# Performance work log

Hardware: AMD Instinct MI355X
Metric: run time of the kernel (lower is better)

The kernel has to match this reference:

```python
import jax, jax.numpy as jnp
import numpy as np

EPS = 1e-5
GROUPS = 32


def setup_inputs() -> dict:
    key = jax.random.key(0)
    ks = jax.random.split(key, 3)
    B, C, H, W = 4, 256, 64, 64
    x = jax.random.normal(ks[0], (B, C, H, W), dtype=jnp.float32)
    gn_w = jnp.ones((C,), dtype=jnp.float32)
    gn_b = jnp.zeros((C,), dtype=jnp.float32)
    qkv_w = jax.random.normal(ks[1], (3 * C, C), dtype=jnp.float32) * (C ** -0.5)
    qkv_b = jnp.zeros((3 * C,), dtype=jnp.float32)
    proj_w = jax.random.normal(ks[2], (C, C), dtype=jnp.float32) * (C ** -0.5)
    proj_b = jnp.zeros((C,), dtype=jnp.float32)
    return {"x": x, "gn_w": gn_w, "gn_b": gn_b, "qkv_w": qkv_w,
            "qkv_b": qkv_b, "proj_w": proj_w, "proj_b": proj_b}


def reference(x, gn_w, gn_b, qkv_w, qkv_b, proj_w, proj_b):
    B, C, H, W = x.shape
    N = H * W
    # GroupNorm over (C//G, H, W) per group
    xg = x.reshape(B, GROUPS, -1)
    mean = xg.mean(axis=-1, keepdims=True)
    var = xg.var(axis=-1, keepdims=True)
    h = ((xg - mean) * jax.lax.rsqrt(var + EPS)).reshape(B, C, H, W)
    h = h * gn_w[None, :, None, None] + gn_b[None, :, None, None]
    # 1x1 conv QKV == channel GEMM
    hf = h.reshape(B, C, N)
    qkv = jnp.einsum('oc,bcn->bon', qkv_w, hf) + qkv_b[None, :, None]
    q, k, v = (qkv[:, :C], qkv[:, C:2 * C], qkv[:, 2 * C:])  # each [B,C,N]
    scale = C ** -0.5
    attn = jax.nn.softmax(jnp.einsum('bcn,bcm->bnm', q, k) * scale, axis=-1)
    out = jnp.einsum('bnm,bcm->bcn', attn, v)  # [B,C,N]
    y = jnp.einsum('oc,bcn->bon', proj_w, out) + proj_b[None, :, None]
    return x + y.reshape(B, C, H, W)
```

## Files before the change

### kernel.cpp

```cpp
#include <hip/hip_runtime.h>
#include <cstdint>
#include <cstddef>

typedef __attribute__((ext_vector_type(8))) short bf16x8;
typedef __attribute__((ext_vector_type(4))) short s16x4;
typedef __attribute__((ext_vector_type(2))) short s16x2;
typedef __attribute__((ext_vector_type(4))) float f32x4;
typedef __attribute__((ext_vector_type(16))) float f32x16;
typedef __attribute__((ext_vector_type(4))) unsigned u32x4;

#define DEVI static __device__ __forceinline__

DEVI short f2bf(float f){
  unsigned u = __builtin_bit_cast(unsigned, f);
  u += 0x7fffu + ((u >> 16) & 1u);
  return (short)(u >> 16);
}
DEVI float bf2f(short s){
  unsigned u = ((unsigned)(unsigned short)s) << 16;
  return __builtin_bit_cast(float, u);
}
DEVI unsigned pack_bf16_rne(float a, float b){
  unsigned ua = __builtin_bit_cast(unsigned, a);
  unsigned ub = __builtin_bit_cast(unsigned, b);
  ua += 0x7fffu + ((ua >> 16) & 1u);
  ub += 0x7fffu + ((ub >> 16) & 1u);
  return (ua >> 16) | (ub & 0xffff0000u);
}

DEVI f32x4 mfma16(bf16x8 a, bf16x8 b, f32x4 c){
  return __builtin_amdgcn_mfma_f32_16x16x32_bf16(a, b, c, 0, 0, 0);
}
DEVI f32x16 mfma32(bf16x8 a, bf16x8 b, f32x16 c){
  return __builtin_amdgcn_mfma_f32_32x32x16_bf16(a, b, c, 0, 0, 0);
}

#define QSC 0.09016844005555897f
#define FIXM 8.0f

__global__ __launch_bounds__(256) void k_conv(const float* __restrict__ wq, const float* __restrict__ wp,
                                              short* __restrict__ wqb, short* __restrict__ wpb){
  int t = blockIdx.x * 256 + threadIdx.x;
  for (int i = t; i < 768 * 256; i += 256 * 256) wqb[i] = f2bf(wq[i]);
  if (t < 256 * 256) wpb[t] = f2bf(wp[t]);
}

__global__ __launch_bounds__(256) void k_stats(const float* __restrict__ x, float2* __restrict__ st){
  int b = blockIdx.x >> 5, g = blockIdx.x & 31;
  const f32x4* p = (const f32x4*)(x + ((size_t)(b * 256 + g * 8)) * 4096);
  float s = 0.f, ss = 0.f;
  for (int i = threadIdx.x; i < 8192; i += 256){
    f32x4 v = p[i];
    s  += v[0] + v[1] + v[2] + v[3];
    ss += v[0]*v[0] + v[1]*v[1] + v[2]*v[2] + v[3]*v[3];
  }
  for (int d = 32; d; d >>= 1){ s += __shfl_down(s, d); ss += __shfl_down(ss, d); }
  __shared__ float a0[4], a1[4];
  int w = threadIdx.x >> 6;
  if ((threadIdx.x & 63) == 0){ a0[w] = s; a1[w] = ss; }
  __syncthreads();
  if (threadIdx.x == 0){
    s = a0[0] + a0[1] + a0[2] + a0[3];
    ss = a1[0] + a1[1] + a1[2] + a1[3];
    float mean = s * (1.f / 32768.f);
    float var = ss * (1.f / 32768.f) - mean * mean;
    st[blockIdx.x] = make_float2(mean, rsqrtf(var + 1e-5f));
  }
}

__global__ __launch_bounds__(256) void k_norm(const float* __restrict__ x, const float2* __restrict__ st,
                                              const float* __restrict__ gw, const float* __restrict__ gb,
                                              short* __restrict__ h_t){
  __shared__ short t[256][66];
  int b = blockIdx.x >> 6;
  int n0 = (blockIdx.x & 63) * 64;
  int tid = threadIdx.x;
  for (int r = 0; r < 16; ++r){
    int idx = tid + r * 256;
    int c = idx >> 4, ch = idx & 15;
    f32x4 v = *(const f32x4*)(x + ((size_t)(b * 256 + c)) * 4096 + n0 + ch * 4);
    float2 s = st[b * 32 + (c >> 3)];
    float wv = gw[c] * s.y;
    float bv = gb[c] - s.x * wv;
    s16x2 p0, p1;
    p0[0] = f2bf(v[0] * wv + bv); p0[1] = f2bf(v[1] * wv + bv);
    p1[0] = f2bf(v[2] * wv + bv); p1[1] = f2bf(v[3] * wv + bv);
    *(s16x2*)&t[c][ch * 4]     = p0;
    *(s16x2*)&t[c][ch * 4 + 2] = p1;
  }
  __syncthreads();
  for (int r = 0; r < 8; ++r){
    int idx = tid + r * 256;
    int n = idx >> 5, cc = idx & 31;
    bf16x8 pk;
    #pragma unroll
    for (int j = 0; j < 8; ++j) pk[j] = t[cc * 8 + j][n];
    *(bf16x8*)(h_t + ((size_t)(b * 4096 + n0 + n)) * 256 + cc * 8) = pk;
  }
}

__global__ __launch_bounds__(256) void k_gemm(const short* __restrict__ A,
                                              const short* __restrict__ Bsrc,
                                              const float* __restrict__ bias,
                                              int mtiles, int mode,
                                              short* __restrict__ q_t, short* __restrict__ k_t,
                                              short* __restrict__ v_,
                                              const float* __restrict__ xres, float* __restrict__ outp)
{
  __shared__ short a_s[128 * 72];
  __shared__ short b_s[128 * 72];
  int t = blockIdx.x;
  int mt = t % mtiles; t /= mtiles;
  int nt = t & 31; int b = t >> 5;
  int o0 = mt * 128, n0 = nt * 128;
  int tid = threadIdx.x;
  int lane = tid & 63, w = tid >> 6;
  int col = lane & 15, quad = lane >> 4;
  int wo = (w >> 1) * 64, wn = (w & 1) * 64;

  f32x4 acc[4][4];
  #pragma unroll
  for (int i = 0; i < 4; ++i)
    #pragma unroll
    for (int j = 0; j < 4; ++j)
      #pragma unroll
      for (int r = 0; r < 4; ++r) acc[i][j][r] = 0.f;

  for (int kk = 0; kk < 4; ++kk){
    int k0 = kk * 64;
    #pragma unroll
    for (int r = 0; r < 4; ++r){
      int idx = tid + r * 256;
      int row = idx >> 3, ch = idx & 7;
      *(bf16x8*)&a_s[row * 72 + ch * 8] = *(const bf16x8*)(A + (size_t)(o0 + row) * 256 + k0 + ch * 8);
      *(bf16x8*)&b_s[row * 72 + ch * 8] = *(const bf16x8*)(Bsrc + ((size_t)(b * 4096 + n0 + row)) * 256 + k0 + ch * 8);
    }
    __syncthreads();
    #pragma unroll
    for (int kc = 0; kc < 2; ++kc){
      bf16x8 af[4], bfr[4];
      #pragma unroll
      for (int i = 0; i < 4; ++i) af[i]  = *(bf16x8*)&a_s[(wo + i * 16 + col) * 72 + kc * 32 + quad * 8];
      #pragma unroll
      for (int j = 0; j < 4; ++j) bfr[j] = *(bf16x8*)&b_s[(wn + j * 16 + col) * 72 + kc * 32 + quad * 8];
      #pragma unroll
      for (int i = 0; i < 4; ++i)
        #pragma unroll
        for (int j = 0; j < 4; ++j)
          acc[i][j] = mfma16(af[i], bfr[j], acc[i][j]);
    }
    __syncthreads();
  }

  float bv[4][4];
  #pragma unroll
  for (int i = 0; i < 4; ++i)
    #pragma unroll
    for (int r = 0; r < 4; ++r) bv[i][r] = bias[o0 + wo + i * 16 + quad * 4 + r];

  if (mode == 0){
    int region = o0 >> 8;
    int obase = (o0 & 255) + wo;
    if (region < 2){
      short* dst = region ? k_t : q_t;
      float sc = region ? 1.0f : QSC;
      #pragma unroll
      for (int i = 0; i < 4; ++i)
        #pragma unroll
        for (int j = 0; j < 4; ++j){
          int n = n0 + wn + j * 16 + col;
          s16x4 pk;
          #pragma unroll
          for (int r = 0; r < 4; ++r) pk[r] = f2bf((acc[i][j][r] + bv[i][r]) * sc);
          *(s16x4*)(dst + ((size_t)(b * 4096 + n)) * 256 + obase + i * 16 + quad * 4) = pk;
        }
    } else {
      #pragma unroll
      for (int i = 0; i < 4; ++i)
        #pragma unroll
        for (int r = 0; r < 4; ++r){
          int oo = obase + i * 16 + quad * 4 + r;
          #pragma unroll
          for (int j = 0; j < 4; ++j){
            int n = n0 + wn + j * 16 + col;
            v_[((size_t)(b * 256 + oo)) * 4096 + n] = f2bf(acc[i][j][r] + bv[i][r]);
          }
        }
    }
  } else {
    #pragma unroll
    for (int i = 0; i < 4; ++i)
      #pragma unroll
      for (int r = 0; r < 4; ++r){
        int oo = o0 + wo + i * 16 + quad * 4 + r;
        #pragma unroll
        for (int j = 0; j < 4; ++j){
          int n = n0 + wn + j * 16 + col;
          size_t off = ((size_t)(b * 256 + oo)) * 4096 + n;
          outp[off] = xres[off] + acc[i][j][r] + bv[i][r];
        }
      }
  }
}

__global__ __launch_bounds__(256, 2) void k_attn(const short* __restrict__ q_t, const short* __restrict__ k_t,
                                                 const short* __restrict__ v_,
                                                 short* __restrict__ o_part, float* __restrict__ lsum)
{
  __shared__ short k_s[32 * 256];
  __shared__ short v_s[256 * 32];
  int idx = blockIdx.x;
  int qt = idx >> 4;
  int chunk = idx & 15;
  int b  = chunk >> 2;
  int ck = chunk & 3;
  int q0 = qt * 128;
  int tid = threadIdx.x, lane = tid & 63, w = tid >> 6;
  int col = lane & 31, h = lane >> 5;

  const short* qp = q_t + ((size_t)(b * 4096 + q0 + w * 32 + col)) * 256 + h * 8;
  bf16x8 qf[16];
  #pragma unroll
  for (int ks2 = 0; ks2 < 16; ++ks2) qf[ks2] = *(const bf16x8*)(qp + ks2 * 16);

  const short* kcb = k_t + ((size_t)(b * 4096 + ck * 1024)) * 256;
  const short* vcb = v_  + ((size_t)b) * 256 * 4096 + ck * 1024;

  int k_r = w * 8 + (lane >> 5);
  int k_p = lane & 31;
  int v_c = w * 64 + (lane >> 2);
  int v_p = lane & 3;

  f32x16 o_acc[8];
  #pragma unroll
  for (int ct = 0; ct < 8; ++ct)
    #pragma unroll
    for (int r = 0; r < 16; ++r) o_acc[ct][r] = 0.f;
  float l_acc = 0.f;

  #pragma unroll 1
  for (int it = 0; it < 32; ++it){
    int m0 = it * 32;
    bf16x8 kst[4], vst[4];
    #pragma unroll
    for (int i = 0; i < 4; ++i){
      kst[i] = *(const bf16x8*)(kcb + (size_t)(m0 + k_r + i * 2) * 256 + k_p * 8);
      vst[i] = *(const bf16x8*)(vcb + (size_t)(v_c + i * 16) * 4096 + m0 + v_p * 8);
    }
    if (it) __syncthreads();
    #pragma unroll
    for (int i = 0; i < 4; ++i){
      int r = k_r + i * 2;
      *(bf16x8*)&k_s[r * 256 + (k_p ^ (r & 7)) * 8] = kst[i];
      int c = v_c + i * 16;
      *(bf16x8*)&v_s[c * 32 + (v_p ^ ((c >> 1) & 3)) * 8] = vst[i];
    }
    __syncthreads();

    f32x16 s;
    #pragma unroll
    for (int r = 0; r < 16; ++r) s[r] = 0.f;
    #pragma unroll
    for (int ks2 = 0; ks2 < 16; ++ks2){
      bf16x8 kb = *(const bf16x8*)&k_s[col * 256 + (((ks2 * 2 + h) ^ (col & 7)) * 8)];
      s = mfma32(kb, qf[ks2], s);
    }

    bf16x8 pa0, pa1;
    {
      float p0 = __builtin_amdgcn_exp2f(s[0] - FIXM);
      float p1 = __builtin_amdgcn_exp2f(s[1] - FIXM);
      float p2 = __builtin_amdgcn_exp2f(s[2] - FIXM);
      float p3 = __builtin_amdgcn_exp2f(s[3] - FIXM);
      float p4 = __builtin_amdgcn_exp2f(s[4] - FIXM);
      float p5 = __builtin_amdgcn_exp2f(s[5] - FIXM);
      float p6 = __builtin_amdgcn_exp2f(s[6] - FIXM);
      float p7 = __builtin_amdgcn_exp2f(s[7] - FIXM);
      l_acc += p0 + p1 + p2 + p3 + p4 + p5 + p6 + p7;
      unsigned A0 = pack_bf16_rne(p0, p1), A1 = pack_bf16_rne(p2, p3);
      unsigned B0 = pack_bf16_rne(p4, p5), B1 = pack_bf16_rne(p6, p7);
      unsigned sA0 = __shfl_xor(A0, 32), sA1 = __shfl_xor(A1, 32);
      unsigned sB0 = __shfl_xor(B0, 32), sB1 = __shfl_xor(B1, 32);
      u32x4 w0;
      w0[0] = h ? sB0 : A0;  w0[1] = h ? sB1 : A1;
      w0[2] = h ? B0 : sA0;  w0[3] = h ? B1 : sA1;
      pa0 = __builtin_bit_cast(bf16x8, w0);
    }
    {
      float p0 = __builtin_amdgcn_exp2f(s[8]  - FIXM);
      float p1 = __builtin_amdgcn_exp2f(s[9]  - FIXM);
      float p2 = __builtin_amdgcn_exp2f(s[10] - FIXM);
      float p3 = __builtin_amdgcn_exp2f(s[11] - FIXM);
      float p4 = __builtin_amdgcn_exp2f(s[12] - FIXM);
      float p5 = __builtin_amdgcn_exp2f(s[13] - FIXM);
      float p6 = __builtin_amdgcn_exp2f(s[14] - FIXM);
      float p7 = __builtin_amdgcn_exp2f(s[15] - FIXM);
      l_acc += p0 + p1 + p2 + p3 + p4 + p5 + p6 + p7;
      unsigned C0 = pack_bf16_rne(p0, p1), C1 = pack_bf16_rne(p2, p3);
      unsigned D0 = pack_bf16_rne(p4, p5), D1 = pack_bf16_rne(p6, p7);
      unsigned sC0 = __shfl_xor(C0, 32), sC1 = __shfl_xor(C1, 32);
      unsigned sD0 = __shfl_xor(D0, 32), sD1 = __shfl_xor(D1, 32);
      u32x4 w1;
      w1[0] = h ? sD0 : C0;  w1[1] = h ? sD1 : C1;
      w1[2] = h ? D0 : sC0;  w1[3] = h ? D1 : sC1;
      pa1 = __builtin_bit_cast(bf16x8, w1);
    }

    #pragma unroll
    for (int ct = 0; ct < 8; ++ct){
      int c = ct * 32 + col;
      int sw = (c >> 1) & 3;
      bf16x8 vf0 = *(const bf16x8*)&v_s[c * 32 + ((h ^ sw) * 8)];
      bf16x8 vf1 = *(const bf16x8*)&v_s[c * 32 + (((2 + h) ^ sw) * 8)];
      o_acc[ct] = mfma32(pa0, vf0, o_acc[ct]);
      o_acc[ct] = mfma32(pa1, vf1, o_acc[ct]);
    }
  }

  short* op = o_part + (((size_t)(ck * 4 + b)) * 4096 + q0 + w * 32) * 256;
  #pragma unroll
  for (int r = 0; r < 16; ++r){
    int q = (r & 3) + 8 * (r >> 2) + 4 * h;
    #pragma unroll
    for (int ct = 0; ct < 8; ++ct)
      op[(size_t)q * 256 + ct * 32 + col] = f2bf(o_acc[ct][r]);
  }
  l_acc += __shfl_xor(l_acc, 32);
  if (h == 0)
    lsum[((size_t)(ck * 4 + b)) * 4096 + q0 + w * 32 + col] = l_acc;
}

__global__ __launch_bounds__(256) void k_comb(const short* __restrict__ o_part, const float* __restrict__ lsum,
                                              short* __restrict__ o_t)
{
  int t = blockIdx.x * 256 + threadIdx.x;
  int row = t >> 5;
  int c8 = (t & 31) * 8;
  float inv = 1.f / (lsum[row] + lsum[16384 + row] + lsum[2 * 16384 + row] + lsum[3 * 16384 + row]);
  size_t base = (size_t)row * 256 + c8;
  const size_t CS = (size_t)16384 * 256;
  bf16x8 a0 = *(const bf16x8*)(o_part + base);
  bf16x8 a1 = *(const bf16x8*)(o_part + CS + base);
  bf16x8 a2 = *(const bf16x8*)(o_part + 2 * CS + base);
  bf16x8 a3 = *(const bf16x8*)(o_part + 3 * CS + base);
  bf16x8 outv;
  #pragma unroll
  for (int j = 0; j < 8; ++j)
    outv[j] = f2bf((bf2f(a0[j]) + bf2f(a1[j]) + bf2f(a2[j]) + bf2f(a3[j])) * inv);
  *(bf16x8*)(o_t + base) = outv;
}

extern "C" void kernel_launch(void* const* d_in, const int* in_sizes, int n_in,
                              void* d_out, int out_size, void* d_ws, size_t ws_size,
                              hipStream_t stream)
{
  const float* x     = (const float*)d_in[0];
  const float* gw    = (const float*)d_in[1];
  const float* gb    = (const float*)d_in[2];
  const float* qkvw  = (const float*)d_in[3];
  const float* qkvb  = (const float*)d_in[4];
  const float* projw = (const float*)d_in[5];
  const float* projb = (const float*)d_in[6];
  float* out = (float*)d_out;

  char* ws = (char*)d_ws;
  float2* stats = (float2*)ws;
  short* wqb = (short*)(ws + 1024);
  short* wpb = (short*)(ws + 1024 + 393216);
  short* h_t = (short*)(ws + 1024 + 393216 + 131072);
  const size_t BIG = (size_t)4 * 4096 * 256;
  short* q_t = h_t + BIG;
  short* k_t = q_t + BIG;
  short* v_  = k_t + BIG;
  short* o_t = v_  + BIG;
  short* o_part = o_t + BIG;
  float* lsum = (float*)(o_part + 4 * BIG);

  k_conv <<<dim3(256),  dim3(256), 0, stream>>>(qkvw, projw, wqb, wpb);
  k_stats<<<dim3(128),  dim3(256), 0, stream>>>(x, stats);
  k_norm <<<dim3(256),  dim3(256), 0, stream>>>(x, stats, gw, gb, h_t);
  k_gemm <<<dim3(768),  dim3(256), 0, stream>>>(wqb, h_t, qkvb, 6, 0, q_t, k_t, v_,
                                                (const float*)nullptr, (float*)nullptr);
  k_attn <<<dim3(512),  dim3(256), 0, stream>>>(q_t, k_t, v_, o_part, lsum);
  k_comb <<<dim3(2048), dim3(256), 0, stream>>>(o_part, lsum, o_t);
  k_gemm <<<dim3(256),  dim3(256), 0, stream>>>(wpb, o_t, projb, 2, 1,
                                                (short*)nullptr, (short*)nullptr, (short*)nullptr,
                                                x, out);
}
```

Baseline: 205.0 us.

## Double-buffer attention K/V tiles with direct global-to-LDS loads

The attention kernel now stages K and V tiles straight from global memory into LDS with global_load_lds, into two ping-pong buffers, so loading tile it+1 overlaps compute on tile it. The swizzle moves from the LDS write side to the per-lane global source address. The QK^T MFMA chain is also split into two independent accumulators to shorten the dependency chain. LDS use doubles to 64KB per block, which may limit the two-blocks-per-CU occupancy target. It also relies on the async LDS loads having landed by the barrier, with no explicit vmcnt wait.

```diff
diff --git a/kernel.cpp b/kernel.cpp
--- a/kernel.cpp
+++ b/kernel.cpp
@@ -26,6 +26,10 @@
   ua += 0x7fffu + ((ua >> 16) & 1u);
   ub += 0x7fffu + ((ub >> 16) & 1u);
   return (ua >> 16) | (ub & 0xffff0000u);
+}
+DEVI void g2l16(const short* g, short* l){
+  __builtin_amdgcn_global_load_lds((const __attribute__((address_space(1))) void*)g,
+                                   (__attribute__((address_space(3))) void*)l, 16, 0, 0);
 }
 
 DEVI f32x4 mfma16(bf16x8 a, bf16x8 b, f32x4 c){
@@ -207,8 +211,8 @@
                                                  const short* __restrict__ v_,
                                                  short* __restrict__ o_part, float* __restrict__ lsum)
 {
-  __shared__ short k_s[32 * 256];
-  __shared__ short v_s[256 * 32];
+  __shared__ short k_s[2][32 * 256];
+  __shared__ short v_s[2][256 * 32];
   int idx = blockIdx.x;
   int qt = idx >> 4;
   int chunk = idx & 15;
@@ -226,10 +230,27 @@
   const short* kcb = k_t + ((size_t)(b * 4096 + ck * 1024)) * 256;
   const short* vcb = v_  + ((size_t)b) * 256 * 4096 + ck * 1024;
 
-  int k_r = w * 8 + (lane >> 5);
-  int k_p = lane & 31;
-  int v_c = w * 64 + (lane >> 2);
-  int v_p = lane & 3;
+  int koff[4], voff[4];
+  #pragma unroll
+  for (int i = 0; i < 4; ++i){
+    int r  = w * 8 + 2 * i + (lane >> 5);
+    koff[i] = r * 256 + (((lane & 31) ^ (r & 7)) * 8);
+    int rv = w * 64 + 16 * i + (lane >> 2);
+    voff[i] = rv * 4096 + (((lane & 3) ^ ((rv >> 1) & 3)) * 8);
+  }
+
+  auto STAGE = [&](int bufi, int itt){
+    const short* kg = kcb + itt * 8192;
+    const short* vg = vcb + itt * 32;
+    short* kl = (short*)k_s[bufi];
+    short* vl = (short*)v_s[bufi];
+    #pragma unroll
+    for (int i = 0; i < 4; ++i)
+      g2l16(kg + koff[i], kl + (w * 8 + 2 * i) * 256);
+    #pragma unroll
+    for (int i = 0; i < 4; ++i)
+      g2l16(vg + voff[i], vl + (w * 64 + 16 * i) * 32);
+  };
 
   f32x16 o_acc[8];
   #pragma unroll
@@ -238,44 +259,39 @@
     for (int r = 0; r < 16; ++r) o_acc[ct][r] = 0.f;
   float l_acc = 0.f;
 
+  STAGE(0, 0);
+  __syncthreads();
+
   #pragma unroll 1
   for (int it = 0; it < 32; ++it){
-    int m0 = it * 32;
-    bf16x8 kst[4], vst[4];
-    #pragma unroll
-    for (int i = 0; i < 4; ++i){
-      kst[i] = *(const bf16x8*)(kcb + (size_t)(m0 + k_r + i * 2) * 256 + k_p * 8);
-      vst[i] = *(const bf16x8*)(vcb + (size_t)(v_c + i * 16) * 4096 + m0 + v_p * 8);
-    }
-    if (it) __syncthreads();
-    #pragma unroll
-    for (int i = 0; i < 4; ++i){
-      int r = k_r + i * 2;
-      *(bf16x8*)&k_s[r * 256 + (k_p ^ (r & 7)) * 8] = kst[i];
-      int c = v_c + i * 16;
-      *(bf16x8*)&v_s[c * 32 + (v_p ^ ((c >> 1) & 3)) * 8] = vst[i];
-    }
-    __syncthreads();
-
-    f32x16 s;
-    #pragma unroll
-    for (int r = 0; r < 16; ++r) s[r] = 0.f;
-    #pragma unroll
-    for (int ks2 = 0; ks2 < 16; ++ks2){
-      bf16x8 kb = *(const bf16x8*)&k_s[col * 256 + (((ks2 * 2 + h) ^ (col & 7)) * 8)];
-      s = mfma32(kb, qf[ks2], s);
-    }
+    int cur = it & 1;
+    if (it < 31) STAGE(cur ^ 1, it + 1);
+    const short* kc = k_s[cur];
+    const short* vc = v_s[cur];
+
+    f32x16 sa, sb;
+    #pragma unroll
+    for (int r = 0; r < 16; ++r){ sa[r] = 0.f; sb[r] = 0.f; }
+    #pragma unroll
+    for (int j = 0; j < 8; ++j){
+      bf16x8 kb0 = *(const bf16x8*)&kc[col * 256 + ((((4 * j)     + h) ^ (col & 7)) * 8)];
+      bf16x8 kb1 = *(const bf16x8*)&kc[col * 256 + ((((4 * j + 2) + h) ^ (col & 7)) * 8)];
+      sa = mfma32(kb0, qf[2 * j],     sa);
+      sb = mfma32(kb1, qf[2 * j + 1], sb);
+    }
+    #pragma unroll
+    for (int r = 0; r < 16; ++r) sa[r] += sb[r];
 
     bf16x8 pa0, pa1;
     {
-      float p0 = __builtin_amdgcn_exp2f(s[0] - FIXM);
-      float p1 = __builtin_amdgcn_exp2f(s[1] - FIXM);
-      float p2 = __builtin_amdgcn_exp2f(s[2] - FIXM);
-      float p3 = __builtin_amdgcn_exp2f(s[3] - FIXM);
-      float p4 = __builtin_amdgcn_exp2f(s[4] - FIXM);
-      float p5 = __builtin_amdgcn_exp2f(s[5] - FIXM);
-      float p6 = __builtin_amdgcn_exp2f(s[6] - FIXM);
-      float p7 = __builtin_amdgcn_exp2f(s[7] - FIXM);
+      float p0 = __builtin_amdgcn_exp2f(sa[0] - FIXM);
+      float p1 = __builtin_amdgcn_exp2f(sa[1] - FIXM);
+      float p2 = __builtin_amdgcn_exp2f(sa[2] - FIXM);
+      float p3 = __builtin_amdgcn_exp2f(sa[3] - FIXM);
+      float p4 = __builtin_amdgcn_exp2f(sa[4] - FIXM);
+      float p5 = __builtin_amdgcn_exp2f(sa[5] - FIXM);
+      float p6 = __builtin_amdgcn_exp2f(sa[6] - FIXM);
+      float p7 = __builtin_amdgcn_exp2f(sa[7] - FIXM);
       l_acc += p0 + p1 + p2 + p3 + p4 + p5 + p6 + p7;
       unsigned A0 = pack_bf16_rne(p0, p1), A1 = pack_bf16_rne(p2, p3);
       unsigned B0 = pack_bf16_rne(p4, p5), B1 = pack_bf16_rne(p6, p7);
@@ -287,14 +303,14 @@
       pa0 = __builtin_bit_cast(bf16x8, w0);
     }
     {
-      float p0 = __builtin_amdgcn_exp2f(s[8]  - FIXM);
-      float p1 = __builtin_amdgcn_exp2f(s[9]  - FIXM);
-      float p2 = __builtin_amdgcn_exp2f(s[10] - FIXM);
-      float p3 = __builtin_amdgcn_exp2f(s[11] - FIXM);
-      float p4 = __builtin_amdgcn_exp2f(s[12] - FIXM);
-      float p5 = __builtin_amdgcn_exp2f(s[13] - FIXM);
-      float p6 = __builtin_amdgcn_exp2f(s[14] - FIXM);
-      float p7 = __builtin_amdgcn_exp2f(s[15] - FIXM);
+      float p0 = __builtin_amdgcn_exp2f(sa[8]  - FIXM);
+      float p1 = __builtin_amdgcn_exp2f(sa[9]  - FIXM);
+      float p2 = __builtin_amdgcn_exp2f(sa[10] - FIXM);
+      float p3 = __builtin_amdgcn_exp2f(sa[11] - FIXM);
+      float p4 = __builtin_amdgcn_exp2f(sa[12] - FIXM);
+      float p5 = __builtin_amdgcn_exp2f(sa[13] - FIXM);
+      float p6 = __builtin_amdgcn_exp2f(sa[14] - FIXM);
+      float p7 = __builtin_amdgcn_exp2f(sa[15] - FIXM);
       l_acc += p0 + p1 + p2 + p3 + p4 + p5 + p6 + p7;
       unsigned C0 = pack_bf16_rne(p0, p1), C1 = pack_bf16_rne(p2, p3);
       unsigned D0 = pack_bf16_rne(p4, p5), D1 = pack_bf16_rne(p6, p7);
@@ -310,11 +326,13 @@
     for (int ct = 0; ct < 8; ++ct){
       int c = ct * 32 + col;
       int sw = (c >> 1) & 3;
-      bf16x8 vf0 = *(const bf16x8*)&v_s[c * 32 + ((h ^ sw) * 8)];
-      bf16x8 vf1 = *(const bf16x8*)&v_s[c * 32 + (((2 + h) ^ sw) * 8)];
+      bf16x8 vf0 = *(const bf16x8*)&vc[c * 32 + ((h ^ sw) * 8)];
+      bf16x8 vf1 = *(const bf16x8*)&vc[c * 32 + (((2 + h) ^ sw) * 8)];
       o_acc[ct] = mfma32(pa0, vf0, o_acc[ct]);
       o_acc[ct] = mfma32(pa1, vf1, o_acc[ct]);
     }
+
+    if (it < 31) __syncthreads();
   }
 
   short* op = o_part + (((size_t)(ck * 4 + b)) * 4096 + q0 + w * 32) * 256;
```

Result: slower. 233.0 us (+13.6%).
